# Performance work log

Measured on AMD Instinct MI355X. Metric: run time of the kernel, lower is better.

## Reference

```python
import jax, jax.numpy as jnp
import numpy as np

V, H, P, L, O = 47, 1024, 4, 3, 47
B, T = 256, 128


def setup_inputs() -> dict:
    key = jax.random.key(0)
    ks = jax.random.split(key, 10)
    s = 1.0 / np.sqrt(H)
    b_ih = jnp.zeros((L, 4 * H), jnp.float32).at[:, H:2 * H].set(1.0)  # forget-gate bias = 1
    return {
        "x": jax.random.randint(ks[0], (B, T), 0, V),
        "properties": jax.random.normal(ks[1], (B, P), jnp.float32),
        "emb": jax.random.normal(ks[2], (V, H), jnp.float32) * s,
        "W_dec": jax.random.normal(ks[3], (O, H), jnp.float32) * s,
        "b_dec": jnp.zeros((O,), jnp.float32),
        "W_ih0": jax.random.normal(ks[4], (4 * H, H + P), jnp.float32) * s,
        "W_ih_rest": jax.random.normal(ks[5], (L - 1, 4 * H, H), jnp.float32) * s,
        "W_hh": jax.random.normal(ks[6], (L, 4 * H, H), jnp.float32) * s,
        "b_ih": b_ih,
        "b_hh": jnp.zeros((L, 4 * H), jnp.float32),
    }


def _lstm_step(x_in, h, c, W_ih, W_hh, b_ih, b_hh):
    # x_in: [B, in_dim]; h, c: [B, H]; gate order i,f,g,o (PyTorch)
    gates = x_in @ W_ih.T + h @ W_hh.T + b_ih + b_hh  # [B, 4H]
    i, f, g, o = jnp.split(gates, 4, axis=-1)
    c_new = jax.nn.sigmoid(f) * c + jax.nn.sigmoid(i) * jnp.tanh(g)
    h_new = jax.nn.sigmoid(o) * jnp.tanh(c_new)
    return h_new, c_new


def reference(x, properties, emb, W_dec, b_dec, W_ih0, W_ih_rest, W_hh, b_ih, b_hh):
    bsz, max_length = x.shape
    h0 = jnp.zeros((L, bsz, H), emb.dtype)
    c0 = jnp.zeros((L, bsz, H), emb.dtype)
    inp0 = emb[jnp.zeros((bsz,), jnp.int32)]  # initial token id 0 -> [B, H]

    def step(carry, _):
        h, c, inp = carry
        x_in = jnp.concatenate([inp, properties], axis=-1)  # [B, H+P]
        hs, cs = [], []
        for l in range(L):
            W_ih_l = W_ih0 if l == 0 else W_ih_rest[l - 1]
            h_l, c_l = _lstm_step(x_in, h[l], c[l], W_ih_l, W_hh[l], b_ih[l], b_hh[l])
            hs.append(h_l); cs.append(c_l)
            x_in = h_l
        logits = x_in @ W_dec.T + b_dec  # [B, O]
        nxt = jnp.argmax(logits, axis=-1)  # greedy decode
        new_carry = (jnp.stack(hs), jnp.stack(cs), emb[nxt])
        return new_carry, logits

    (h, c, _), logits_seq = jax.lax.scan(step, (h0, c0, inp0), None, length=max_length)
    outputs = jnp.transpose(logits_seq, (1, 0, 2))  # [B, T, O]
    return outputs, h, c
```

## Files before the change

kernel.cpp:

```cpp
#include <hip/hip_runtime.h>
#include <hip/hip_bf16.h>
#include <cstdint>
#include <cstddef>


#define BB 256
#define TT 128
#define OO 47

typedef __attribute__((ext_vector_type(8))) _Float16 f16x8;
typedef __attribute__((ext_vector_type(4))) float f32x4;

#define CBUF_B   0u
#define HF32_B   3145728u
#define BCOMB_B  9437184u
#define EHI_B    9486336u
#define ELO_B    10043392u
#define HS_B     10600448u
#define W_B      16891904u
#define WS_NEEDED 118603776u

#define BARRIER() asm volatile("s_barrier" ::: "memory")
#define WAITV(n)  asm volatile("s_waitcnt vmcnt(" #n ")" ::: "memory")
#define WAITLGKM0() asm volatile("s_waitcnt lgkmcnt(0)" ::: "memory")

__device__ __forceinline__ float fsig(float x) {
  return 1.0f / (1.0f + exp2f(-1.4426950408889634f * x));
}
__device__ __forceinline__ float ftanhf(float x) {
  float e = exp2f(2.8853900817779268f * x);
  return 1.0f - 2.0f / (e + 1.0f);
}
__device__ __forceinline__ unsigned short f16b(_Float16 h) {
  union { _Float16 f; unsigned short u; } c; c.f = h; return c.u;
}
__device__ __forceinline__ void gld16(const void* g, void* l) {
  __builtin_amdgcn_global_load_lds(
      (const __attribute__((address_space(1))) unsigned int*)g,
      (__attribute__((address_space(3))) unsigned int*)l, 16, 0, 0);
}
__device__ __forceinline__ size_t slab_addr(int grp, int NCH, int k, int r) {
  return ((size_t)grp * NCH + (k >> 5)) * 512 + ((k >> 4) & 1) * 256 +
         ((k >> 3) & 1) * 128 + r * 8 + (k & 7);
}

__global__ void k_zero(float* p, int n) {
  int i = blockIdx.x * blockDim.x + threadIdx.x;
  int stride = gridDim.x * blockDim.x;
  for (; i < n; i += stride) p[i] = 0.0f;
}

__global__ void k_binit(float* bc, const float* __restrict__ bih,
                        const float* __restrict__ bhh) {
  int i = blockIdx.x * blockDim.x + threadIdx.x;
  if (i < 12288) bc[i] = bih[i] + bhh[i];
}

__global__ void k_prepw(const float* __restrict__ src, unsigned short* dhi,
                        unsigned short* dlo, int K, int NCH) {
  const int nrow = blockIdx.x;
  const int ngrp = nrow >> 4, rr = nrow & 15;
  const float* s = src + (size_t)nrow * K;
  for (int k = threadIdx.x; k < NCH * 32; k += blockDim.x) {
    float val = (k < K) ? s[k] : 0.0f;
    _Float16 h16 = (_Float16)val;
    _Float16 l16 = (_Float16)((val - (float)h16) * 2048.0f);
    size_t a = slab_addr(ngrp, NCH, k, rr);
    dhi[a] = f16b(h16);
    dlo[a] = f16b(l16);
  }
}

__global__ void k_einit(unsigned short* ehi, unsigned short* elo,
                        const float* __restrict__ emb,
                        const float* __restrict__ props) {
  const int b = blockIdx.x;
  for (int j = threadIdx.x; j < 1088; j += blockDim.x) {
    float val = (j < 1024) ? emb[j] : (j < 1028 ? props[b * 4 + (j - 1024)] : 0.0f);
    _Float16 h16 = (_Float16)val;
    _Float16 l16 = (_Float16)((val - (float)h16) * 2048.0f);
    size_t a = slab_addr(b >> 4, 34, j, b & 15);
    ehi[a] = f16b(h16);
    elo[a] = f16b(l16);
  }
}

__global__ __launch_bounds__(512, 2) void k_layer(
    const char* __restrict__ xhi, const char* __restrict__ xlo,
    int NCHXmem, int nstX,
    const char* __restrict__ hhi, const char* __restrict__ hlo,
    const char* __restrict__ wxhi, const char* __restrict__ wxlo,
    const char* __restrict__ whhi, const char* __restrict__ whlo,
    const float* __restrict__ bcomb, float* __restrict__ cbuf,
    float* __restrict__ hdstf, unsigned short* __restrict__ hshi,
    unsigned short* __restrict__ hslo) {
  __shared__ char LBUF[131072];
  const int tid = threadIdx.x;
  const int lane = tid & 63, wid = tid >> 6;
  const int nt = blockIdx.x & 63;
  const int mt = blockIdx.x >> 6;
  const int m0 = mt << 6, h0c = nt << 4;
  const int nst = (nstX > 16) ? nstX : 16;

  const int sIsB = wid >> 2, sHalfW = (wid >> 1) & 1, sPrec = wid & 1;
  const int sNch = sHalfW ? 16 : nstX;
  const int sNmem = sHalfW ? 32 : NCHXmem;
  const char* sbase[4];
  {
    const char* t0;
    if (!sIsB) t0 = sHalfW ? (sPrec ? hlo : hhi) : (sPrec ? xlo : xhi);
    else       t0 = sHalfW ? (sPrec ? whlo : whhi) : (sPrec ? wxlo : wxhi);
#pragma unroll
    for (int i = 0; i < 4; ++i) {
      int grp = sIsB ? (i * 64 + nt) : (mt * 4 + i);
      sbase[i] = t0 + (size_t)grp * sNmem * 1024 + (size_t)lane * 16;
    }
  }
  const int ldsoff0 = (sIsB << 15) + (sHalfW << 14) + (sPrec << 13);
  auto stage = [&](int s, int bufbase) {
    char* ldst = LBUF + bufbase + ldsoff0;
    const size_t so = (size_t)s * 2048;
#pragma unroll
    for (int i = 0; i < 4; ++i) {
      gld16(sbase[i] + so, ldst + (i << 10));
      gld16(sbase[i] + so + 1024, ldst + 4096 + (i << 10));
    }
  };

  const int wHalf = wid >> 2, q = wid & 3;
  const int mb = (q >> 1) << 1, nbb = (q & 1) << 1;
  const int waveNst = wHalf ? 16 : nstX;

  f32x4 accH[4], accL[4];
#pragma unroll
  for (int i = 0; i < 4; ++i) {
    accH[i] = f32x4{0.f, 0.f, 0.f, 0.f};
    accL[i] = f32x4{0.f, 0.f, 0.f, 0.f};
  }

  stage(0, 0);
  stage(1, 65536);

  for (int s = 0; s < nst; ++s) {
    const int bufb = (s & 1) << 16;
    if (s + 1 < sNch) { WAITV(8); }
    else              { WAITV(0); }
    BARRIER();

    if (s < waveNst) {
      const char* A0 = LBUF + bufb + (wHalf << 14);
      const char* B0 = LBUF + bufb + 32768 + (wHalf << 14);
#pragma unroll
      for (int kc = 0; kc < 2; ++kc) {
        const int kco = kc << 12;
        f16x8 ah[2], al[2], bh[2], bl[2];
#pragma unroll
        for (int r = 0; r < 2; ++r) {
          ah[r] = *(const f16x8*)(A0 + kco + ((mb + r) << 10) + (lane << 4));
          al[r] = *(const f16x8*)(A0 + 8192 + kco + ((mb + r) << 10) + (lane << 4));
        }
#pragma unroll
        for (int c = 0; c < 2; ++c) {
          bh[c] = *(const f16x8*)(B0 + kco + ((nbb + c) << 10) + (lane << 4));
          bl[c] = *(const f16x8*)(B0 + 8192 + kco + ((nbb + c) << 10) + (lane << 4));
        }
        __builtin_amdgcn_s_setprio(1);
#pragma unroll
        for (int r = 0; r < 2; ++r)
#pragma unroll
          for (int c = 0; c < 2; ++c) {
            int ix = r * 2 + c;
            accH[ix] = __builtin_amdgcn_mfma_f32_16x16x32_f16(ah[r], bh[c], accH[ix], 0, 0, 0);
            accL[ix] = __builtin_amdgcn_mfma_f32_16x16x32_f16(al[r], bh[c], accL[ix], 0, 0, 0);
            accL[ix] = __builtin_amdgcn_mfma_f32_16x16x32_f16(ah[r], bl[c], accL[ix], 0, 0, 0);
          }
        __builtin_amdgcn_s_setprio(0);
      }
    }

    WAITLGKM0();
    BARRIER();
    if (s + 2 < sNch) stage(s + 2, bufb);
  }

  BARRIER();
  float* GH = (float*)LBUF;
  float* GL = GH + 64 * 68;
  const int mrow0 = ((q >> 1) << 5) + ((lane >> 4) << 2);
  const int ncol0 = ((q & 1) << 5) + (lane & 15);
  if (wHalf == 0) {
#pragma unroll
    for (int r = 0; r < 2; ++r)
#pragma unroll
      for (int c = 0; c < 2; ++c) {
        f32x4 aH = accH[r * 2 + c], aL = accL[r * 2 + c];
        int mr = mrow0 + r * 16, nc = ncol0 + c * 16;
#pragma unroll
        for (int i = 0; i < 4; ++i) {
          GH[(mr + i) * 68 + nc] = aH[i];
          GL[(mr + i) * 68 + nc] = aL[i];
        }
      }
  }
  __syncthreads();
  if (wHalf == 1) {
#pragma unroll
    for (int r = 0; r < 2; ++r)
#pragma unroll
      for (int c = 0; c < 2; ++c) {
        f32x4 aH = accH[r * 2 + c], aL = accL[r * 2 + c];
        int mr = mrow0 + r * 16, nc = ncol0 + c * 16;
#pragma unroll
        for (int i = 0; i < 4; ++i) {
          GH[(mr + i) * 68 + nc] += aH[i];
          GL[(mr + i) * 68 + nc] += aL[i];
        }
      }
  }
  __syncthreads();

  const float LSC = 1.0f / 2048.0f;
#pragma unroll
  for (int e = 0; e < 2; ++e) {
    int ci = tid * 2 + e;
    int bl_ = ci >> 4, hh = ci & 15;
    int b = m0 + bl_, hcol = h0c + hh;
    float xi = GH[bl_ * 68 + hh]      + GL[bl_ * 68 + hh]      * LSC + bcomb[hcol];
    float xf = GH[bl_ * 68 + 16 + hh] + GL[bl_ * 68 + 16 + hh] * LSC + bcomb[1024 + hcol];
    float xg = GH[bl_ * 68 + 32 + hh] + GL[bl_ * 68 + 32 + hh] * LSC + bcomb[2048 + hcol];
    float xo = GH[bl_ * 68 + 48 + hh] + GL[bl_ * 68 + 48 + hh] * LSC + bcomb[3072 + hcol];
    size_t cidx = (size_t)b * 1024 + hcol;
    float cn = fsig(xf) * cbuf[cidx] + fsig(xi) * ftanhf(xg);
    float hn = fsig(xo) * ftanhf(cn);
    cbuf[cidx] = cn;
    hdstf[cidx] = hn;
    _Float16 h16 = (_Float16)hn;
    _Float16 l16 = (_Float16)((hn - (float)h16) * 2048.0f);
    size_t sa = slab_addr(b >> 4, 32, hcol, b & 15);
    hshi[sa] = f16b(h16);
    hslo[sa] = f16b(l16);
  }
}

__global__ __launch_bounds__(256) void k_decode(
    const float* __restrict__ h2, const float* __restrict__ Wdec,
    const float* __restrict__ bdec, const float* __restrict__ emb,
    float* __restrict__ out, unsigned short* __restrict__ ehi,
    unsigned short* __restrict__ elo, int t) {
  __shared__ float P[4][64];
  __shared__ int tokS;
  const int b = blockIdx.x;
  const int w = threadIdx.x >> 6, lane = threadIdx.x & 63;
  const float* hrow = h2 + (size_t)b * 1024 + w * 256;
  float part = 0.f;
  if (lane < OO) {
    const float* wrow = Wdec + (size_t)lane * 1024 + w * 256;
    float p0 = 0.f, p1 = 0.f, p2 = 0.f, p3 = 0.f;
    for (int k = 0; k < 256; k += 16) {
      float4 w0 = *(const float4*)(wrow + k);      float4 h0v = *(const float4*)(hrow + k);
      float4 w1 = *(const float4*)(wrow + k + 4);  float4 h1v = *(const float4*)(hrow + k + 4);
      float4 w2 = *(const float4*)(wrow + k + 8);  float4 h2v = *(const float4*)(hrow + k + 8);
      float4 w3 = *(const float4*)(wrow + k + 12); float4 h3v = *(const float4*)(hrow + k + 12);
      p0 += w0.x * h0v.x + w0.y * h0v.y + w0.z * h0v.z + w0.w * h0v.w;
      p1 += w1.x * h1v.x + w1.y * h1v.y + w1.z * h1v.z + w1.w * h1v.w;
      p2 += w2.x * h2v.x + w2.y * h2v.y + w2.z * h2v.z + w2.w * h2v.w;
      p3 += w3.x * h3v.x + w3.y * h3v.y + w3.z * h3v.z + w3.w * h3v.w;
    }
    part = (p0 + p1) + (p2 + p3);
  }
  P[w][lane] = part;
  __syncthreads();
  if (w == 0) {
    float logit = -3.0e38f;
    if (lane < OO)
      logit = P[0][lane] + P[1][lane] + P[2][lane] + P[3][lane] + bdec[lane];
    float vv = logit;
    int idx = (lane < OO) ? lane : 1000;
#pragma unroll
    for (int m = 1; m < 64; m <<= 1) {
      float v2 = __shfl_xor(vv, m, 64);
      int i2 = __shfl_xor(idx, m, 64);
      if (v2 > vv || (v2 == vv && i2 < idx)) { vv = v2; idx = i2; }
    }
    if (lane < OO) out[(size_t)b * (TT * OO) + t * OO + lane] = logit;
    if (lane == 0) tokS = idx;
  }
  __syncthreads();
  if (t < TT - 1) {
    const float* erow = emb + (size_t)tokS * 1024;
    float4 ev = ((const float4*)erow)[threadIdx.x];
    float vals[4] = {ev.x, ev.y, ev.z, ev.w};
#pragma unroll
    for (int r = 0; r < 4; ++r) {
      int j = threadIdx.x * 4 + r;
      _Float16 h16 = (_Float16)vals[r];
      _Float16 l16 = (_Float16)((vals[r] - (float)h16) * 2048.0f);
      size_t a = slab_addr(b >> 4, 34, j, b & 15);
      ehi[a] = f16b(h16);
      elo[a] = f16b(l16);
    }
  }
}

__global__ void k_final(const float* __restrict__ hf, const float* __restrict__ cb,
                        float* __restrict__ out) {
  int i = blockIdx.x * blockDim.x + threadIdx.x;
  int stride = gridDim.x * blockDim.x;
  const int HBASE = BB * TT * OO;
  for (; i < 2 * 786432; i += stride) {
    if (i < 786432) {
      int l = i >> 18, r = i & 262143;
      out[HBASE + i] = hf[(size_t)(l * 2 + 0) * 262144 + r];
    } else {
      int j = i - 786432;
      out[HBASE + 786432 + j] = cb[j];
    }
  }
}

#define O_EBUF  0
#define O_HPB   270336
#define O_CBUF  1843200
#define O_BCOMB 2629632
#define O_WSN   2641920
#define O_HP(l, p) (O_HPB + ((l) * 2 + (p)) * 262144)

__global__ void k_initO(float* ws, const float* __restrict__ props,
                        const float* __restrict__ emb,
                        const float* __restrict__ bih,
                        const float* __restrict__ bhh) {
  int i = blockIdx.x * blockDim.x + threadIdx.x;
  if (i < 270336) {
    int b = i / 1056, j = i % 1056;
    float v = 0.0f;
    if (j < 1024) v = emb[j];
    else if (j < 1028) v = props[b * 4 + (j - 1024)];
    ws[O_EBUF + i] = v;
  } else if (i < 270336 + 12288) {
    int j = i - 270336;
    ws[O_BCOMB + j] = bih[j] + bhh[j];
  }
}

__global__ __launch_bounds__(512, 2) void k_layerO(
    const float* __restrict__ xsrc, int xs, int Kx, int nst0,
    const float* __restrict__ hsrc,
    const float* __restrict__ Wx, int wxs,
    const float* __restrict__ Wh,
    const float* __restrict__ bcomb, float* __restrict__ cbuf,
    float* __restrict__ hdst) {
  __shared__ char LBUF[65536];
  const int tid = threadIdx.x;
  const int lane = tid & 63, wid = tid >> 6;
  const int sw = ((blockIdx.x & 7) << 5) + (blockIdx.x >> 3);
  const int mt = sw & 3, nt = sw >> 2;
  const int m0 = mt << 6, h0c = nt << 4;
  const int nstMax = (nst0 > 32) ? nst0 : 32;
  const int tile = tid >> 7;
  const int tt = tid & 127;
  const int srow = tt >> 1;
  const int kseg = (tt & 1) << 4;
  const int isB = tile >> 1, sHalf = tile & 1;
  const int myNst = sHalf ? 32 : nst0;
  const float* grow;
  int KactB = 0x7fffffff;
  if (!isB) {
    grow = sHalf ? (hsrc + (size_t)(m0 + srow) * 1024)
                 : (xsrc + (size_t)(m0 + srow) * xs);
  } else {
    int nrow = ((srow >> 4) << 10) + h0c + (srow & 15);
    grow = sHalf ? (Wh + (size_t)nrow * 1024) : (Wx + (size_t)nrow * wxs);
    KactB = sHalf ? 1024 : Kx;
  }
  const int wbase = ((srow >> 4) << 10) + ((tt & 1) << 9) + ((srow & 15) << 4);
  const int ssec = (isB << 14) + (sHalf << 13);
  const int wHalf = wid >> 2, q = wid & 3;
  const int mb = (q >> 1) << 1, nbb = (q & 1) << 1;
  const int waveNst = wHalf ? 32 : nst0;
  const int secAr = (wHalf << 13);
  const int secBr = 16384 + (wHalf << 13);
  f32x4 accH[4], accL[4];
#pragma unroll
  for (int i = 0; i < 4; ++i) {
    accH[i] = f32x4{0.f, 0.f, 0.f, 0.f};
    accL[i] = f32x4{0.f, 0.f, 0.f, 0.f};
  }
  float4 v[4];
  auto load_regs = [&](int s) {
    const int kl = (s << 5) + kseg;
    const float4* p = (const float4*)(grow + kl);
#pragma unroll
    for (int qq = 0; qq < 4; ++qq) {
      int kk = kl + qq * 4;
      if (kk < KactB) v[qq] = p[qq];
      else v[qq] = float4{0.f, 0.f, 0.f, 0.f};
    }
  };
  auto cvt_write = [&](int buf) {
    char* base = LBUF + buf * 32768 + ssec + wbase;
#pragma unroll
    for (int g = 0; g < 2; ++g) {
      float fs[8] = {v[2*g].x, v[2*g].y, v[2*g].z, v[2*g].w,
                     v[2*g+1].x, v[2*g+1].y, v[2*g+1].z, v[2*g+1].w};
      f16x8 hvv, lvv;
#pragma unroll
      for (int j = 0; j < 8; ++j) {
        _Float16 h16 = (_Float16)fs[j];
        lvv[j] = (_Float16)((fs[j] - (float)h16) * 2048.0f);
        hvv[j] = h16;
      }
      *(f16x8*)(base + g * 256) = hvv;
      *(f16x8*)(base + g * 256 + 4096) = lvv;
    }
  };
  load_regs(0);
  cvt_write(0);
  __syncthreads();
  for (int s = 0; s < nstMax; ++s) {
    const int cur = s & 1, nxt = cur ^ 1;
    const bool doStage = (s + 1 < myNst);
    if (doStage) load_regs(s + 1);
    if (s < waveNst) {
      const char* A0 = LBUF + cur * 32768 + secAr;
      const char* B0 = LBUF + cur * 32768 + secBr;
      f16x8 ah[2], al[2], bh[2], bl[2];
#pragma unroll
      for (int r = 0; r < 2; ++r) {
        ah[r] = *(const f16x8*)(A0 + ((mb + r) << 10) + (lane << 4));
        al[r] = *(const f16x8*)(A0 + 4096 + ((mb + r) << 10) + (lane << 4));
      }
#pragma unroll
      for (int c = 0; c < 2; ++c) {
        bh[c] = *(const f16x8*)(B0 + ((nbb + c) << 10) + (lane << 4));
        bl[c] = *(const f16x8*)(B0 + 4096 + ((nbb + c) << 10) + (lane << 4));
      }
#pragma unroll
      for (int r = 0; r < 2; ++r)
#pragma unroll
        for (int c = 0; c < 2; ++c) {
          int ix = r * 2 + c;
          accH[ix] = __builtin_amdgcn_mfma_f32_16x16x32_f16(ah[r], bh[c], accH[ix], 0, 0, 0);
          accL[ix] = __builtin_amdgcn_mfma_f32_16x16x32_f16(al[r], bh[c], accL[ix], 0, 0, 0);
          accL[ix] = __builtin_amdgcn_mfma_f32_16x16x32_f16(ah[r], bl[c], accL[ix], 0, 0, 0);
        }
    }
    if (doStage) cvt_write(nxt);
    __syncthreads();
  }
  float* GH = (float*)LBUF;
  float* GL = GH + 64 * 68;
  const int mrow0 = ((q >> 1) << 5) + ((lane >> 4) << 2);
  const int ncol0 = ((q & 1) << 5) + (lane & 15);
  if (wHalf == 0) {
#pragma unroll
    for (int r = 0; r < 2; ++r)
#pragma unroll
      for (int c = 0; c < 2; ++c) {
        f32x4 aHh = accH[r * 2 + c], aLl = accL[r * 2 + c];
        int mr = mrow0 + r * 16, nc = ncol0 + c * 16;
#pragma unroll
        for (int i = 0; i < 4; ++i) { GH[(mr + i) * 68 + nc] = aHh[i]; GL[(mr + i) * 68 + nc] = aLl[i]; }
      }
  }
  __syncthreads();
  if (wHalf == 1) {
#pragma unroll
    for (int r = 0; r < 2; ++r)
#pragma unroll
      for (int c = 0; c < 2; ++c) {
        f32x4 aHh = accH[r * 2 + c], aLl = accL[r * 2 + c];
        int mr = mrow0 + r * 16, nc = ncol0 + c * 16;
#pragma unroll
        for (int i = 0; i < 4; ++i) { GH[(mr + i) * 68 + nc] += aHh[i]; GL[(mr + i) * 68 + nc] += aLl[i]; }
      }
  }
  __syncthreads();
  const float LSC = 1.0f / 2048.0f;
#pragma unroll
  for (int e = 0; e < 2; ++e) {
    int ci = tid * 2 + e;
    int bl_ = ci >> 4, hh = ci & 15;
    int b = m0 + bl_, hcol = h0c + hh;
    float xi = GH[bl_ * 68 + hh]      + GL[bl_ * 68 + hh]      * LSC + bcomb[hcol];
    float xf = GH[bl_ * 68 + 16 + hh] + GL[bl_ * 68 + 16 + hh] * LSC + bcomb[1024 + hcol];
    float xg = GH[bl_ * 68 + 32 + hh] + GL[bl_ * 68 + 32 + hh] * LSC + bcomb[2048 + hcol];
    float xo = GH[bl_ * 68 + 48 + hh] + GL[bl_ * 68 + 48 + hh] * LSC + bcomb[3072 + hcol];
    size_t cidx = (size_t)b * 1024 + hcol;
    float cn = fsig(xf) * cbuf[cidx] + fsig(xi) * ftanhf(xg);
    float hn = fsig(xo) * ftanhf(cn);
    cbuf[cidx] = cn;
    hdst[cidx] = hn;
  }
}

__global__ __launch_bounds__(64) void k_decodeO(
    const float* __restrict__ h2, const float* __restrict__ Wdec,
    const float* __restrict__ bdec, const float* __restrict__ emb,
    float* __restrict__ out, float* __restrict__ ebuf, int t) {
  const int b = blockIdx.x, lane = threadIdx.x;
  const float* hrow = h2 + (size_t)b * 1024;
  float logit = 0.f;
  if (lane < OO) {
    const float* wrow = Wdec + (size_t)lane * 1024;
    float p0 = 0.f, p1 = 0.f, p2 = 0.f, p3 = 0.f;
    for (int k = 0; k < 1024; k += 16) {
      float4 w0 = *(const float4*)(wrow + k);      float4 h0v = *(const float4*)(hrow + k);
      float4 w1 = *(const float4*)(wrow + k + 4);  float4 h1v = *(const float4*)(hrow + k + 4);
      float4 w2 = *(const float4*)(wrow + k + 8);  float4 h2v = *(const float4*)(hrow + k + 8);
      float4 w3 = *(const float4*)(wrow + k + 12); float4 h3v = *(const float4*)(hrow + k + 12);
      p0 += w0.x * h0v.x + w0.y * h0v.y + w0.z * h0v.z + w0.w * h0v.w;
      p1 += w1.x * h1v.x + w1.y * h1v.y + w1.z * h1v.z + w1.w * h1v.w;
      p2 += w2.x * h2v.x + w2.y * h2v.y + w2.z * h2v.z + w2.w * h2v.w;
      p3 += w3.x * h3v.x + w3.y * h3v.y + w3.z * h3v.z + w3.w * h3v.w;
    }
    logit = ((p0 + p1) + (p2 + p3)) + bdec[lane];
  }
  float vv = (lane < OO) ? logit : -3.0e38f;
  int idx = (lane < OO) ? lane : 1000;
#pragma unroll
  for (int m = 1; m < 64; m <<= 1) {
    float v2 = __shfl_xor(vv, m, 64);
    int i2 = __shfl_xor(idx, m, 64);
    if (v2 > vv || (v2 == vv && i2 < idx)) { vv = v2; idx = i2; }
  }
  if (lane < OO) out[(size_t)b * (TT * OO) + t * OO + lane] = logit;
  if (t < TT - 1) {
    const float* erow = emb + (size_t)idx * 1024;
#pragma unroll
    for (int i = 0; i < 16; ++i) {
      int h = i * 64 + lane;
      ebuf[(size_t)b * 1056 + h] = erow[h];
    }
  }
}

__global__ void k_finalO(const float* __restrict__ ws, float* __restrict__ out) {
  int i = blockIdx.x * blockDim.x + threadIdx.x;
  int stride = gridDim.x * blockDim.x;
  const int HBASE = BB * TT * OO;
  for (; i < 2 * 786432; i += stride) {
    if (i < 786432) {
      int l = i >> 18, r = i & 262143;
      out[HBASE + i] = ws[O_HP(l, 0) + r];
    } else {
      int j = i - 786432;
      out[HBASE + 786432 + j] = ws[O_CBUF + j];
    }
  }
}

extern "C" void kernel_launch(void* const* d_in, const int* in_sizes, int n_in,
                              void* d_out, int out_size, void* d_ws, size_t ws_size,
                              hipStream_t stream) {
  const float* props = (const float*)d_in[1];
  const float* emb   = (const float*)d_in[2];
  const float* Wdec  = (const float*)d_in[3];
  const float* bdec  = (const float*)d_in[4];
  const float* Wih0  = (const float*)d_in[5];
  const float* Wihr  = (const float*)d_in[6];
  const float* Whh   = (const float*)d_in[7];
  const float* bih   = (const float*)d_in[8];
  const float* bhh   = (const float*)d_in[9];
  float* out = (float*)d_out;

  if (ws_size >= (size_t)WS_NEEDED) {
    char* base = (char*)d_ws;
    float* cb = (float*)(base + CBUF_B);
    float* hf = (float*)(base + HF32_B);
    float* bc = (float*)(base + BCOMB_B);
    unsigned short* Ehi = (unsigned short*)(base + EHI_B);
    unsigned short* Elo = (unsigned short*)(base + ELO_B);
    auto HS = [&](int l, int p, int prec) {
      return (unsigned short*)(base + HS_B + (size_t)((l * 2 + p) * 2 + prec) * 524288u);
    };
    unsigned short* Wp[12];
    {
      size_t off = W_B;
      Wp[0] = (unsigned short*)(base + off); off += 8912896u;
      Wp[1] = (unsigned short*)(base + off); off += 8912896u;
      for (int i = 2; i < 12; ++i) { Wp[i] = (unsigned short*)(base + off); off += 8388608u; }
    }

    k_zero<<<2048, 256, 0, stream>>>((float*)base, 2359296);
    k_zero<<<2048, 256, 0, stream>>>((float*)(base + HS_B), 1572864);
    k_binit<<<48, 256, 0, stream>>>(bc, bih, bhh);
    k_einit<<<256, 256, 0, stream>>>(Ehi, Elo, emb, props);
    k_prepw<<<4096, 256, 0, stream>>>(Wih0, Wp[0], Wp[1], 1028, 34);
    k_prepw<<<4096, 256, 0, stream>>>(Whh,                           Wp[2], Wp[3], 1024, 32);
    k_prepw<<<4096, 256, 0, stream>>>(Wihr,                          Wp[4], Wp[5], 1024, 32);
    k_prepw<<<4096, 256, 0, stream>>>(Whh + (size_t)4096 * 1024,     Wp[6], Wp[7], 1024, 32);
    k_prepw<<<4096, 256, 0, stream>>>(Wihr + (size_t)4096 * 1024,    Wp[8], Wp[9], 1024, 32);
    k_prepw<<<4096, 256, 0, stream>>>(Whh + (size_t)2 * 4096 * 1024, Wp[10], Wp[11], 1024, 32);

    for (int t = 0; t < TT; ++t) {
      const int p = t & 1, pn = p ^ 1;
      k_layer<<<256, 512, 0, stream>>>(
          (const char*)Ehi, (const char*)Elo, 34, 17,
          (const char*)HS(0, p, 0), (const char*)HS(0, p, 1),
          (const char*)Wp[0], (const char*)Wp[1],
          (const char*)Wp[2], (const char*)Wp[3],
          bc, cb, hf + (size_t)(0 * 2 + pn) * 262144,
          HS(0, pn, 0), HS(0, pn, 1));
      k_layer<<<256, 512, 0, stream>>>(
          (const char*)HS(0, pn, 0), (const char*)HS(0, pn, 1), 32, 16,
          (const char*)HS(1, p, 0), (const char*)HS(1, p, 1),
          (const char*)Wp[4], (const char*)Wp[5],
          (const char*)Wp[6], (const char*)Wp[7],
          bc + 4096, cb + 262144, hf + (size_t)(1 * 2 + pn) * 262144,
          HS(1, pn, 0), HS(1, pn, 1));
      k_layer<<<256, 512, 0, stream>>>(
          (const char*)HS(1, pn, 0), (const char*)HS(1, pn, 1), 32, 16,
          (const char*)HS(2, p, 0), (const char*)HS(2, p, 1),
          (const char*)Wp[8], (const char*)Wp[9],
          (const char*)Wp[10], (const char*)Wp[11],
          bc + 8192, cb + 524288, hf + (size_t)(2 * 2 + pn) * 262144,
          HS(2, pn, 0), HS(2, pn, 1));
      k_decode<<<256, 256, 0, stream>>>(hf + (size_t)(2 * 2 + pn) * 262144,
                                        Wdec, bdec, emb, out, Ehi, Elo, t);
    }
    k_final<<<2048, 256, 0, stream>>>(hf, cb, out);
  } else {
    float* ws = (float*)d_ws;
    float* E  = ws + O_EBUF;
    float* cb = ws + O_CBUF;
    float* bc = ws + O_BCOMB;
    k_zero<<<2048, 256, 0, stream>>>(ws, O_WSN);
    k_initO<<<1104, 256, 0, stream>>>(ws, props, emb, bih, bhh);
    for (int t = 0; t < TT; ++t) {
      const int p = t & 1;
      k_layerO<<<256, 512, 0, stream>>>(E, 1056, 1028, 33, ws + O_HP(0, p),
                                        Wih0, 1028, Whh, bc, cb, ws + O_HP(0, p ^ 1));
      k_layerO<<<256, 512, 0, stream>>>(ws + O_HP(0, p ^ 1), 1024, 1024, 32,
                                        ws + O_HP(1, p), Wihr, 1024,
                                        Whh + (size_t)4096 * 1024,
                                        bc + 4096, cb + 262144, ws + O_HP(1, p ^ 1));
      k_layerO<<<256, 512, 0, stream>>>(ws + O_HP(1, p ^ 1), 1024, 1024, 32,
                                        ws + O_HP(2, p),
                                        Wihr + (size_t)4096 * 1024, 1024,
                                        Whh + (size_t)2 * 4096 * 1024,
                                        bc + 8192, cb + 524288, ws + O_HP(2, p ^ 1));
      k_decodeO<<<256, 64, 0, stream>>>(ws + O_HP(2, p ^ 1), Wdec, bdec, emb, out, E, t);
    }
    k_finalO<<<2048, 256, 0, stream>>>(ws, out);
  }
}
```

Before: 9.959 ms.

## Use 128-row tiles with sequential K in LSTM layer kernel, drop split-K

Each LSTM layer step now runs as 128 blocks of 1024 threads. Each block computes a 128x64 gate tile and walks the x-part and h-part of K in one sequential pipelined loop. Previously the x and h contributions were split across wave halves and reduced through LDS. The larger M tile halves how often each weight slice is streamed from memory, and removing split-K removes the cross-half reduction and its extra barrier. In exchange, half as many blocks are launched (fewer than the CU count) and the serial K loop is about twice as long per block, which may reduce parallelism and latency hiding.

```diff
diff --git a/kernel.cpp b/kernel.cpp
--- a/kernel.cpp
+++ b/kernel.cpp
@@ -85,7 +85,7 @@
   }
 }
 
-__global__ __launch_bounds__(512, 2) void k_layer(
+__global__ __launch_bounds__(1024, 4) void k_layer(
     const char* __restrict__ xhi, const char* __restrict__ xlo,
     int NCHXmem, int nstX,
     const char* __restrict__ hhi, const char* __restrict__ hlo,
@@ -94,141 +94,120 @@
     const float* __restrict__ bcomb, float* __restrict__ cbuf,
     float* __restrict__ hdstf, unsigned short* __restrict__ hshi,
     unsigned short* __restrict__ hslo) {
-  __shared__ char LBUF[131072];
+  __shared__ char LBUF[98304];
   const int tid = threadIdx.x;
   const int lane = tid & 63, wid = tid >> 6;
   const int nt = blockIdx.x & 63;
   const int mt = blockIdx.x >> 6;
-  const int m0 = mt << 6, h0c = nt << 4;
-  const int nst = (nstX > 16) ? nstX : 16;
-
-  const int sIsB = wid >> 2, sHalfW = (wid >> 1) & 1, sPrec = wid & 1;
-  const int sNch = sHalfW ? 16 : nstX;
-  const int sNmem = sHalfW ? 32 : NCHXmem;
-  const char* sbase[4];
-  {
-    const char* t0;
-    if (!sIsB) t0 = sHalfW ? (sPrec ? hlo : hhi) : (sPrec ? xlo : xhi);
-    else       t0 = sHalfW ? (sPrec ? whlo : whhi) : (sPrec ? wxlo : wxhi);
-#pragma unroll
-    for (int i = 0; i < 4; ++i) {
-      int grp = sIsB ? (i * 64 + nt) : (mt * 4 + i);
-      sbase[i] = t0 + (size_t)grp * sNmem * 1024 + (size_t)lane * 16;
-    }
-  }
-  const int ldsoff0 = (sIsB << 15) + (sHalfW << 14) + (sPrec << 13);
+  const int m0 = mt << 7, h0c = nt << 4;
+  const int nst = nstX + 16;
+
+  const char* xb[3];
+  const char* hb[3];
+  int ldoff[3];
+#pragma unroll
+  for (int i = 0; i < 3; ++i) {
+    int j = wid * 3 + i;
+    if (j < 32) {
+      int prec = j & 1, ksub = (j >> 1) & 1, grp = j >> 2;
+      int grpg = mt * 8 + grp;
+      const char* xs = prec ? xlo : xhi;
+      const char* hs = prec ? hlo : hhi;
+      xb[i] = xs + ((size_t)grpg * NCHXmem + ksub) * 1024 + (size_t)lane * 16;
+      hb[i] = hs + ((size_t)grpg * 32 + ksub) * 1024 + (size_t)lane * 16;
+      ldoff[i] = (prec << 14) | (ksub << 13) | (grp << 10);
+    } else {
+      int jj = j - 32;
+      int prec = jj & 1, ksub = (jj >> 1) & 1, bgrp = jj >> 2;
+      int grpg = bgrp * 64 + nt;
+      const char* xs = prec ? wxlo : wxhi;
+      const char* hs = prec ? whlo : whhi;
+      xb[i] = xs + ((size_t)grpg * NCHXmem + ksub) * 1024 + (size_t)lane * 16;
+      hb[i] = hs + ((size_t)grpg * 32 + ksub) * 1024 + (size_t)lane * 16;
+      ldoff[i] = 32768 | (prec << 13) | (ksub << 12) | (bgrp << 10);
+    }
+  }
   auto stage = [&](int s, int bufbase) {
-    char* ldst = LBUF + bufbase + ldsoff0;
-    const size_t so = (size_t)s * 2048;
-#pragma unroll
-    for (int i = 0; i < 4; ++i) {
-      gld16(sbase[i] + so, ldst + (i << 10));
-      gld16(sbase[i] + so + 1024, ldst + 4096 + (i << 10));
-    }
+    const int part = (s >= nstX);
+    const size_t koff = (size_t)(part ? (s - nstX) : s) * 2048;
+    char* ldst = LBUF + bufbase;
+#pragma unroll
+    for (int i = 0; i < 3; ++i)
+      gld16((part ? hb[i] : xb[i]) + koff, ldst + ldoff[i]);
   };
 
-  const int wHalf = wid >> 2, q = wid & 3;
-  const int mb = (q >> 1) << 1, nbb = (q & 1) << 1;
-  const int waveNst = wHalf ? 16 : nstX;
-
-  f32x4 accH[4], accL[4];
-#pragma unroll
-  for (int i = 0; i < 4; ++i) {
+  const int wm = wid >> 2, wn = wid & 3;
+
+  f32x4 accH[2], accL[2];
+#pragma unroll
+  for (int i = 0; i < 2; ++i) {
     accH[i] = f32x4{0.f, 0.f, 0.f, 0.f};
     accL[i] = f32x4{0.f, 0.f, 0.f, 0.f};
   }
 
   stage(0, 0);
-  stage(1, 65536);
+  stage(1, 49152);
 
   for (int s = 0; s < nst; ++s) {
-    const int bufb = (s & 1) << 16;
-    if (s + 1 < sNch) { WAITV(8); }
-    else              { WAITV(0); }
+    const int bufb = (s & 1) ? 49152 : 0;
+    if (s + 1 < nst) { WAITV(3); }
+    else             { WAITV(0); }
     BARRIER();
 
-    if (s < waveNst) {
-      const char* A0 = LBUF + bufb + (wHalf << 14);
-      const char* B0 = LBUF + bufb + 32768 + (wHalf << 14);
-#pragma unroll
-      for (int kc = 0; kc < 2; ++kc) {
-        const int kco = kc << 12;
-        f16x8 ah[2], al[2], bh[2], bl[2];
-#pragma unroll
-        for (int r = 0; r < 2; ++r) {
-          ah[r] = *(const f16x8*)(A0 + kco + ((mb + r) << 10) + (lane << 4));
-          al[r] = *(const f16x8*)(A0 + 8192 + kco + ((mb + r) << 10) + (lane << 4));
+    {
+      const char* Bf = LBUF + bufb;
+#pragma unroll
+      for (int ksub = 0; ksub < 2; ++ksub) {
+        f16x8 ah[2], al[2], bh, bl;
+#pragma unroll
+        for (int mf = 0; mf < 2; ++mf) {
+          int grp = wm * 2 + mf;
+          ah[mf] = *(const f16x8*)(Bf + ((0 << 14) | (ksub << 13) | (grp << 10)) + (lane << 4));
+          al[mf] = *(const f16x8*)(Bf + ((1 << 14) | (ksub << 13) | (grp << 10)) + (lane << 4));
         }
-#pragma unroll
-        for (int c = 0; c < 2; ++c) {
-          bh[c] = *(const f16x8*)(B0 + kco + ((nbb + c) << 10) + (lane << 4));
-          bl[c] = *(const f16x8*)(B0 + 8192 + kco + ((nbb + c) << 10) + (lane << 4));
+        bh = *(const f16x8*)(Bf + (32768 | (0 << 13) | (ksub << 12) | (wn << 10)) + (lane << 4));
+        bl = *(const f16x8*)(Bf + (32768 | (1 << 13) | (ksub << 12) | (wn << 10)) + (lane << 4));
+        __builtin_amdgcn_s_setprio(1);
+#pragma unroll
+        for (int mf = 0; mf < 2; ++mf) {
+          accH[mf] = __builtin_amdgcn_mfma_f32_16x16x32_f16(ah[mf], bh, accH[mf], 0, 0, 0);
+          accL[mf] = __builtin_amdgcn_mfma_f32_16x16x32_f16(al[mf], bh, accL[mf], 0, 0, 0);
+          accL[mf] = __builtin_amdgcn_mfma_f32_16x16x32_f16(ah[mf], bl, accL[mf], 0, 0, 0);
         }
-        __builtin_amdgcn_s_setprio(1);
-#pragma unroll
-        for (int r = 0; r < 2; ++r)
-#pragma unroll
-          for (int c = 0; c < 2; ++c) {
-            int ix = r * 2 + c;
-            accH[ix] = __builtin_amdgcn_mfma_f32_16x16x32_f16(ah[r], bh[c], accH[ix], 0, 0, 0);
-            accL[ix] = __builtin_amdgcn_mfma_f32_16x16x32_f16(al[r], bh[c], accL[ix], 0, 0, 0);
-            accL[ix] = __builtin_amdgcn_mfma_f32_16x16x32_f16(ah[r], bl[c], accL[ix], 0, 0, 0);
-          }
         __builtin_amdgcn_s_setprio(0);
       }
     }
 
     WAITLGKM0();
     BARRIER();
-    if (s + 2 < sNch) stage(s + 2, bufb);
+    if (s + 2 < nst) stage(s + 2, bufb);
   }
 
   BARRIER();
-  float* GH = (float*)LBUF;
-  float* GL = GH + 64 * 68;
-  const int mrow0 = ((q >> 1) << 5) + ((lane >> 4) << 2);
-  const int ncol0 = ((q & 1) << 5) + (lane & 15);
-  if (wHalf == 0) {
-#pragma unroll
-    for (int r = 0; r < 2; ++r)
-#pragma unroll
-      for (int c = 0; c < 2; ++c) {
-        f32x4 aH = accH[r * 2 + c], aL = accL[r * 2 + c];
-        int mr = mrow0 + r * 16, nc = ncol0 + c * 16;
-#pragma unroll
-        for (int i = 0; i < 4; ++i) {
-          GH[(mr + i) * 68 + nc] = aH[i];
-          GL[(mr + i) * 68 + nc] = aL[i];
-        }
+  float* G = (float*)LBUF;
+  const float LSC = 1.0f / 2048.0f;
+  {
+    const int col = wn * 16 + (lane & 15);
+    const int r0 = wm * 32 + ((lane >> 4) << 2);
+#pragma unroll
+    for (int mf = 0; mf < 2; ++mf)
+#pragma unroll
+      for (int i = 0; i < 4; ++i) {
+        int row = r0 + mf * 16 + i;
+        G[row * 68 + col] = accH[mf][i] + accL[mf][i] * LSC;
       }
   }
   __syncthreads();
-  if (wHalf == 1) {
-#pragma unroll
-    for (int r = 0; r < 2; ++r)
-#pragma unroll
-      for (int c = 0; c < 2; ++c) {
-        f32x4 aH = accH[r * 2 + c], aL = accL[r * 2 + c];
-        int mr = mrow0 + r * 16, nc = ncol0 + c * 16;
-#pragma unroll
-        for (int i = 0; i < 4; ++i) {
-          GH[(mr + i) * 68 + nc] += aH[i];
-          GL[(mr + i) * 68 + nc] += aL[i];
-        }
-      }
-  }
-  __syncthreads();
-
-  const float LSC = 1.0f / 2048.0f;
+
 #pragma unroll
   for (int e = 0; e < 2; ++e) {
     int ci = tid * 2 + e;
-    int bl_ = ci >> 4, hh = ci & 15;
-    int b = m0 + bl_, hcol = h0c + hh;
-    float xi = GH[bl_ * 68 + hh]      + GL[bl_ * 68 + hh]      * LSC + bcomb[hcol];
-    float xf = GH[bl_ * 68 + 16 + hh] + GL[bl_ * 68 + 16 + hh] * LSC + bcomb[1024 + hcol];
-    float xg = GH[bl_ * 68 + 32 + hh] + GL[bl_ * 68 + 32 + hh] * LSC + bcomb[2048 + hcol];
-    float xo = GH[bl_ * 68 + 48 + hh] + GL[bl_ * 68 + 48 + hh] * LSC + bcomb[3072 + hcol];
+    int row = ci >> 4, hh = ci & 15;
+    int b = m0 + row, hcol = h0c + hh;
+    float xi = G[row * 68 + hh]      + bcomb[hcol];
+    float xf = G[row * 68 + 16 + hh] + bcomb[1024 + hcol];
+    float xg = G[row * 68 + 32 + hh] + bcomb[2048 + hcol];
+    float xo = G[row * 68 + 48 + hh] + bcomb[3072 + hcol];
     size_t cidx = (size_t)b * 1024 + hcol;
     float cn = fsig(xf) * cbuf[cidx] + fsig(xi) * ftanhf(xg);
     float hn = fsig(xo) * ftanhf(cn);
@@ -594,21 +573,21 @@
 
     for (int t = 0; t < TT; ++t) {
       const int p = t & 1, pn = p ^ 1;
-      k_layer<<<256, 512, 0, stream>>>(
+      k_layer<<<128, 1024, 0, stream>>>(
           (const char*)Ehi, (const char*)Elo, 34, 17,
           (const char*)HS(0, p, 0), (const char*)HS(0, p, 1),
           (const char*)Wp[0], (const char*)Wp[1],
           (const char*)Wp[2], (const char*)Wp[3],
           bc, cb, hf + (size_t)(0 * 2 + pn) * 262144,
           HS(0, pn, 0), HS(0, pn, 1));
-      k_layer<<<256, 512, 0, stream>>>(
+      k_layer<<<128, 1024, 0, stream>>>(
           (const char*)HS(0, pn, 0), (const char*)HS(0, pn, 1), 32, 16,
           (const char*)HS(1, p, 0), (const char*)HS(1, p, 1),
           (const char*)Wp[4], (const char*)Wp[5],
           (const char*)Wp[6], (const char*)Wp[7],
           bc + 4096, cb + 262144, hf + (size_t)(1 * 2 + pn) * 262144,
           HS(1, pn, 0), HS(1, pn, 1));
-      k_layer<<<256, 512, 0, stream>>>(
+      k_layer<<<128, 1024, 0, stream>>>(
           (const char*)HS(1, pn, 0), (const char*)HS(1, pn, 1), 32, 16,
           (const char*)HS(2, p, 0), (const char*)HS(2, p, 1),
           (const char*)Wp[8], (const char*)Wp[9],
```

After: 14.19 ms. 1.42x slower.
